# Kernel optimization log

Measured on AMD Instinct MI355X. Metric: run time of the kernel, lower is better.

## Reference

```python
import jax, jax.numpy as jnp
import numpy as np

B, LQ, LD, H, DIM, PF = 16, 64, 2048, 1024, 128, 4
MAXK = LD // PF + 1  # static upper bound on num clusters (valid_len <= LD)


def setup_inputs() -> dict:
    key = jax.random.key(0)
    k1, k2, k3, k4 = jax.random.split(key, 4)
    return {
        "q_hidden": jax.random.normal(k1, (B, LQ, H), jnp.float32),
        "d_hidden": jax.random.normal(k2, (B, LD, H), jnp.float32),
        "W": jax.random.normal(k3, (H, DIM), jnp.float32) * (1.0 / np.sqrt(H)),  # xavier-ish
        "b": jnp.zeros((DIM,), jnp.float32),
        "q_mask": jnp.ones((B, LQ), jnp.int32),
        "d_mask": jnp.ones((B, LD), jnp.int32),
        "labels": jax.random.randint(k4, (B, LD), 0, MAXK, dtype=jnp.int32),
        "pooling_factor": PF,
    }


def _encode(hidden, W, b, mask):
    # proj -> L2 normalize -> zero out padded tokens
    r = hidden @ W + b
    r = r / jnp.clip(jnp.linalg.norm(r, axis=-1, keepdims=True), 1e-12)
    return r * mask[..., None].astype(r.dtype)


def _pool(d_repr, d_mask, labels, pf):
    # segment-mean per batch sample, cluster labels supplied externally
    Bn, L, D = d_repr.shape
    max_k = L // pf + 1  # static
    valid = jnp.clip(d_mask.sum(-1), 2, None)          # [B]
    k = valid // pf + 1                                 # per-sample num clusters
    lab = jnp.where(d_mask > 0, labels % k[:, None], max_k)  # invalid tokens -> dummy seg
    seg = lambda vals, idx: jax.ops.segment_sum(vals, idx, num_segments=max_k + 1)
    sums = jax.vmap(seg)(d_repr, lab)[:, :max_k]                          # [B,K,D]
    counts = jax.vmap(seg)(jnp.where(d_mask > 0, 1.0, 0.0), lab)[:, :max_k]
    means = sums / jnp.clip(counts, 1.0)[..., None]
    means = means / jnp.clip(jnp.linalg.norm(means, axis=-1, keepdims=True), 1e-12)
    pad_mask = jnp.arange(max_k)[None, :] < k[:, None]                    # [B,K]
    return means * pad_mask[..., None], pad_mask


def reference(q_hidden, d_hidden, W, b, q_mask, d_mask, labels, pooling_factor):
    q = _encode(q_hidden, W, b, q_mask)            # [B,LQ,DIM]
    d = _encode(d_hidden, W, b, d_mask)            # [B,LD,DIM]
    d_pool, pmask = _pool(d, d_mask, labels, pooling_factor)  # [B,K,DIM]
    sim = jnp.einsum('bqd,bkd->bqk', q, d_pool)
    sim = jnp.where(pmask[:, None, :], sim, -1e4)
    score = (sim.max(-1) * q_mask.astype(sim.dtype)).sum(-1)  # maxsum per pair
    return score
```

## Files before the change

kernel.cpp:

```cpp
#include <hip/hip_runtime.h>
#include <hip/hip_bf16.h>

#define BB    16
#define LQ    64
#define LD    2048
#define HH    1024
#define DIM   128
#define MAXK  513
#define DGRID 512
#define QGRID 16
#define RSP   16

typedef __attribute__((ext_vector_type(8))) short short8;
typedef __attribute__((ext_vector_type(4))) float f32x4;

__device__ __forceinline__ float b2f(ushort u) {
    union { float f; unsigned int u32; } c; c.u32 = ((unsigned int)u) << 16; return c.f;
}
__device__ __forceinline__ ushort f2b_rn(float f) {
    unsigned int x = __float_as_uint(f);
    return (ushort)((x + 0x7fffu + ((x >> 16) & 1u)) >> 16);
}

__device__ __forceinline__ void gld16(void* lds, const void* g) {
    __builtin_amdgcn_global_load_lds(
        (const __attribute__((address_space(1))) unsigned int*)g,
        (__attribute__((address_space(3))) unsigned int*)lds,
        16, 0, 0);
}

__global__ __launch_bounds__(256) void prep_kb_kernel(
    const float* __restrict__ W,
    const int*   __restrict__ d_mask,
    const int*   __restrict__ pf,
    ushort*      __restrict__ Wt_hi,
    ushort*      __restrict__ Wt_lo,
    int*         __restrict__ kvals)
{
    __shared__ int red[4];
    int bid = blockIdx.x, t = threadIdx.x;
    if (bid < 512) {
        int idx = bid * 256 + t;
        int h = idx >> 7;
        int n = idx & 127;
        float x = W[idx];
        ushort hi = f2b_rn(x);
        float r = x - b2f(hi);
        Wt_hi[n * HH + h] = hi;
        Wt_lo[n * HH + h] = f2b_rn(r);
    } else {
        int b = bid - 512;
        int lane = t & 63, wave = t >> 6;
        int s = 0;
        for (int i = t; i < LD; i += 256) s += (d_mask[b * LD + i] > 0) ? 1 : 0;
        #pragma unroll
        for (int m = 1; m < 64; m <<= 1) s += __shfl_xor(s, m);
        if (lane == 0) red[wave] = s;
        __syncthreads();
        if (t == 0) {
            int v = red[0] + red[1] + red[2] + red[3];
            if (v < 2) v = 2;
            int pfv = pf[0];
            if (pfv < 1 || pfv > LD) pfv = 4;
            kvals[b] = v / pfv + 1;
        }
    }
}

__global__ __launch_bounds__(256, 3) void encode_kernel(
    const float*  __restrict__ Xd,
    const float*  __restrict__ Xq,
    const ushort* __restrict__ Wt_hi,
    const ushort* __restrict__ Wt_lo,
    const float*  __restrict__ bias,
    const int*    __restrict__ mask_d,
    const int*    __restrict__ mask_q,
    const int*    __restrict__ labels,
    const int*    __restrict__ kvals,
    float*        __restrict__ sums,
    float*        __restrict__ q_repr)
{
    __shared__ __align__(16) uint4 buf[2][1536];

    const int t = threadIdx.x;
    const int w = t >> 6, lane = t & 63;
    const int m16 = lane & 15, quad = lane >> 4;
    const int l8 = lane & 7, lr = lane >> 3;
    const int g = l8 ^ lr;

    const bool isq = blockIdx.x >= DGRID;
    const float* X = isq ? Xq : Xd;
    const long row0 = isq ? (long)(blockIdx.x - DGRID) * 64 : (long)blockIdx.x * 64;

    const float* gA0 = X + (row0 + w * 16 + 0 + lr) * HH + g * 4;
    const float* gA1 = X + (row0 + w * 16 + 8 + lr) * HH + g * 4;
    const ushort* bsel = (g & 4) ? Wt_lo : Wt_hi;
    const ushort* gB0 = bsel + ((w * 4 + 0) * 8 + lr) * HH + (g & 3) * 8;
    const ushort* gB1 = bsel + ((w * 4 + 1) * 8 + lr) * HH + (g & 3) * 8;
    const ushort* gB2 = bsel + ((w * 4 + 2) * 8 + lr) * HH + (g & 3) * 8;
    const ushort* gB3 = bsel + ((w * 4 + 3) * 8 + lr) * HH + (g & 3) * 8;

    f32x4 acc[8];
    #pragma unroll
    for (int j = 0; j < 8; ++j) acc[j] = (f32x4){0.f, 0.f, 0.f, 0.f};

    {
        gld16(&buf[0][(w * 2 + 0) * 64], gA0);
        gld16(&buf[0][(w * 2 + 1) * 64], gA1);
        gld16(&buf[0][512 + (w * 4 + 0) * 64], gB0);
        gld16(&buf[0][512 + (w * 4 + 1) * 64], gB1);
        gld16(&buf[0][512 + (w * 4 + 2) * 64], gB2);
        gld16(&buf[0][512 + (w * 4 + 3) * 64], gB3);
    }

    const int sw = m16 & 7;
    const int abase = (w * 16 + m16) * 8;

    for (int c = 0; c < 32; ++c) {
        __syncthreads();
        const int cur = c & 1;

        if (c < 31) {
            const int nxt = cur ^ 1;
            const int ko = (c + 1) * 32;
            gld16(&buf[nxt][(w * 2 + 0) * 64], gA0 + ko);
            gld16(&buf[nxt][(w * 2 + 1) * 64], gA1 + ko);
            gld16(&buf[nxt][512 + (w * 4 + 0) * 64], gB0 + ko);
            gld16(&buf[nxt][512 + (w * 4 + 1) * 64], gB1 + ko);
            gld16(&buf[nxt][512 + (w * 4 + 2) * 64], gB2 + ko);
            gld16(&buf[nxt][512 + (w * 4 + 3) * 64], gB3 + ko);
        }

        float4 va0 = *(const float4*)&buf[cur][abase + ((2 * quad) ^ sw)];
        float4 va1 = *(const float4*)&buf[cur][abase + ((2 * quad + 1) ^ sw)];
        float av[8];
        *(float4*)(av) = va0; *(float4*)(av + 4) = va1;
        short8 ah, al;
        #pragma unroll
        for (int j = 0; j < 8; ++j) {
            unsigned int ux = __float_as_uint(av[j]);
            ah[j] = (short)(ux >> 16);
            float hif = __uint_as_float(ux & 0xffff0000u);
            al[j] = (short)(__float_as_uint(av[j] - hif) >> 16);
        }

        #pragma unroll
        for (int ct = 0; ct < 8; ++ct) {
            const int bbase = 512 + (ct * 16 + m16) * 8;
            short8 bh = *(const short8*)&buf[cur][bbase + (quad ^ sw)];
            short8 bl = *(const short8*)&buf[cur][bbase + ((quad + 4) ^ sw)];
            acc[ct] = __builtin_amdgcn_mfma_f32_16x16x32_bf16(ah, bh, acc[ct], 0, 0, 0);
            acc[ct] = __builtin_amdgcn_mfma_f32_16x16x32_bf16(al, bh, acc[ct], 0, 0, 0);
            acc[ct] = __builtin_amdgcn_mfma_f32_16x16x32_bf16(ah, bl, acc[ct], 0, 0, 0);
        }
    }

    float bia[8];
    #pragma unroll
    for (int ct = 0; ct < 8; ++ct) bia[ct] = bias[ct * 16 + m16];

    #pragma unroll
    for (int r = 0; r < 4; ++r) {
        long rowg = row0 + w * 16 + quad * 4 + r;
        float v[8];
        float ss = 0.f;
        #pragma unroll
        for (int ct = 0; ct < 8; ++ct) {
            v[ct] = acc[ct][r] + bia[ct];
            ss += v[ct] * v[ct];
        }
        ss += __shfl_xor(ss, 1);
        ss += __shfl_xor(ss, 2);
        ss += __shfl_xor(ss, 4);
        ss += __shfl_xor(ss, 8);
        float scale = 1.0f / fmaxf(sqrtf(ss), 1e-12f);

        if (isq) {
            scale *= (float)mask_q[rowg];
            #pragma unroll
            for (int ct = 0; ct < 8; ++ct)
                q_repr[rowg * DIM + ct * 16 + m16] = v[ct] * scale;
        } else {
            if (mask_d[rowg] > 0) {
                int b = (int)(rowg >> 11);
                int seg = labels[rowg] % kvals[b];
                float* sp = sums + ((long)b * MAXK + seg) * DIM + m16;
                #pragma unroll
                for (int ct = 0; ct < 8; ++ct)
                    atomicAdd(sp + ct * 16, v[ct] * scale);
            }
        }
    }
}

__global__ __launch_bounds__(256) void simmax_kernel(
    const float* __restrict__ q_repr,
    const float* __restrict__ sums,
    const int*   __restrict__ kvals,
    const int*   __restrict__ q_mask,
    float*       __restrict__ out)
{
    __shared__ float qs[4 * 132];
    __shared__ float red[4][4];
    int b = blockIdx.x >> 4, rs = blockIdx.x & 15;
    int t = threadIdx.x, w = t >> 6, lane = t & 63;

    for (int i = t; i < 4 * DIM; i += 256) {
        int r = i >> 7, d = i & 127;
        qs[r * 132 + d] = q_repr[((long)b * LQ + rs * 4 + r) * DIM + d];
    }
    __syncthreads();

    int kb = kvals[b];
    float mx[4];
    #pragma unroll
    for (int r = 0; r < 4; ++r) mx[r] = -1e4f;

    for (int kk = t; kk < MAXK; kk += 256) {
        const float4* dp = (const float4*)(sums + ((long)b * MAXK + kk) * DIM);
        float dot[4];
        #pragma unroll
        for (int r = 0; r < 4; ++r) dot[r] = 0.f;
        float ss = 0.f;
        for (int d4 = 0; d4 < 32; ++d4) {
            float4 c = dp[d4];
            ss += c.x * c.x + c.y * c.y + c.z * c.z + c.w * c.w;
            #pragma unroll
            for (int r = 0; r < 4; ++r) {
                float4 q = *(const float4*)(&qs[r * 132 + d4 * 4]);
                dot[r] += q.x * c.x + q.y * c.y + q.z * c.z + q.w * c.w;
            }
        }
        float inv = (ss > 1e-24f) ? rsqrtf(ss) : 0.f;
        bool valid = kk < kb;
        #pragma unroll
        for (int r = 0; r < 4; ++r) {
            float sim = valid ? dot[r] * inv : -1e4f;
            mx[r] = fmaxf(mx[r], sim);
        }
    }

    #pragma unroll
    for (int r = 0; r < 4; ++r) {
        float v = mx[r];
        v = fmaxf(v, __shfl_xor(v, 1));
        v = fmaxf(v, __shfl_xor(v, 2));
        v = fmaxf(v, __shfl_xor(v, 4));
        v = fmaxf(v, __shfl_xor(v, 8));
        v = fmaxf(v, __shfl_xor(v, 16));
        v = fmaxf(v, __shfl_xor(v, 32));
        mx[r] = v;
    }
    if (lane == 0) {
        #pragma unroll
        for (int r = 0; r < 4; ++r) red[w][r] = mx[r];
    }
    __syncthreads();
    if (t < 4) {
        float m = fmaxf(fmaxf(red[0][t], red[1][t]), fmaxf(red[2][t], red[3][t]));
        m *= (float)q_mask[b * LQ + rs * 4 + t];
        atomicAdd(&out[b], m);
    }
}

extern "C" void kernel_launch(void* const* d_in, const int* in_sizes, int n_in,
                              void* d_out, int out_size, void* d_ws, size_t ws_size,
                              hipStream_t stream) {
    const float* q_hidden = (const float*)d_in[0];
    const float* d_hidden = (const float*)d_in[1];
    const float* W        = (const float*)d_in[2];
    const float* bias     = (const float*)d_in[3];
    const int*   q_mask   = (const int*)d_in[4];
    const int*   d_mask   = (const int*)d_in[5];
    const int*   labels   = (const int*)d_in[6];
    const int*   pf       = (const int*)d_in[7];

    float* ws     = (float*)d_ws;
    float* q_repr = ws;
    float* sums   = q_repr + (long)BB * LQ * DIM;
    int*   kvals  = (int*)(sums + (long)BB * MAXK * DIM);
    ushort* Wt_hi = (ushort*)(kvals + 16);
    ushort* Wt_lo = Wt_hi + (long)DIM * HH;

    hipMemsetAsync(sums, 0, (size_t)BB * MAXK * DIM * sizeof(float), stream);
    hipMemsetAsync(d_out, 0, (size_t)out_size * sizeof(float), stream);

    prep_kb_kernel<<<512 + BB, 256, 0, stream>>>(W, d_mask, pf, Wt_hi, Wt_lo, kvals);
    encode_kernel<<<DGRID + QGRID, 256, 0, stream>>>(d_hidden, q_hidden, Wt_hi, Wt_lo,
                                                     bias, d_mask, q_mask, labels, kvals,
                                                     sums, q_repr);
    simmax_kernel<<<BB * RSP, 256, 0, stream>>>(q_repr, sums, kvals, q_mask, (float*)d_out);
}
```

Measured before the change: 291.5 us.

## Drop W low-part split, shrink encode tiles, and move simmax to MFMA

W is now kept as a single bf16 copy, so each k-step of the encode GEMM issues two MFMAs instead of three. The encode tile drops to 32 rows, which doubles the grid and raises the occupancy target to 4 blocks, and the row norm is combined through shared memory. The similarity-max stage becomes a bf16 MFMA GEMM over 64-cluster chunks with split-precision queries, writing partial maxima that a small final kernel reduces without atomics. Dropping W's low part and quantising the cluster sums to bf16 lowers precision and may put error near the tolerance.

```diff
diff --git a/kernel.cpp b/kernel.cpp
--- a/kernel.cpp
+++ b/kernel.cpp
@@ -7,9 +7,9 @@
 #define HH    1024
 #define DIM   128
 #define MAXK  513
-#define DGRID 512
-#define QGRID 16
-#define RSP   16
+#define SCH   9
+#define DGRID 1024
+#define QGRID 32
 
 typedef __attribute__((ext_vector_type(8))) short short8;
 typedef __attribute__((ext_vector_type(4))) float f32x4;
@@ -33,8 +33,7 @@
     const float* __restrict__ W,
     const int*   __restrict__ d_mask,
     const int*   __restrict__ pf,
-    ushort*      __restrict__ Wt_hi,
-    ushort*      __restrict__ Wt_lo,
+    ushort*      __restrict__ Wt,
     int*         __restrict__ kvals)
 {
     __shared__ int red[4];
@@ -43,11 +42,7 @@
         int idx = bid * 256 + t;
         int h = idx >> 7;
         int n = idx & 127;
-        float x = W[idx];
-        ushort hi = f2b_rn(x);
-        float r = x - b2f(hi);
-        Wt_hi[n * HH + h] = hi;
-        Wt_lo[n * HH + h] = f2b_rn(r);
+        Wt[n * HH + h] = f2b_rn(W[idx]);
     } else {
         int b = bid - 512;
         int lane = t & 63, wave = t >> 6;
@@ -67,11 +62,10 @@
     }
 }
 
-__global__ __launch_bounds__(256, 3) void encode_kernel(
+__global__ __launch_bounds__(256, 4) void encode_kernel(
     const float*  __restrict__ Xd,
     const float*  __restrict__ Xq,
-    const ushort* __restrict__ Wt_hi,
-    const ushort* __restrict__ Wt_lo,
+    const ushort* __restrict__ Wt,
     const float*  __restrict__ bias,
     const int*    __restrict__ mask_d,
     const int*    __restrict__ mask_q,
@@ -80,41 +74,36 @@
     float*        __restrict__ sums,
     float*        __restrict__ q_repr)
 {
-    __shared__ __align__(16) uint4 buf[2][1536];
+    __shared__ __align__(16) uint4 buf[2][768];
+    __shared__ float ssh[32][2];
+
+    const int bid = blockIdx.x;
+    const bool isq = bid >= DGRID;
+    const float* X = isq ? Xq : Xd;
+    const long row0 = isq ? (long)(bid - DGRID) * 32 : (long)bid * 32;
 
     const int t = threadIdx.x;
     const int w = t >> 6, lane = t & 63;
     const int m16 = lane & 15, quad = lane >> 4;
-    const int l8 = lane & 7, lr = lane >> 3;
-    const int g = l8 ^ lr;
-
-    const bool isq = blockIdx.x >= DGRID;
-    const float* X = isq ? Xq : Xd;
-    const long row0 = isq ? (long)(blockIdx.x - DGRID) * 64 : (long)blockIdx.x * 64;
-
-    const float* gA0 = X + (row0 + w * 16 + 0 + lr) * HH + g * 4;
-    const float* gA1 = X + (row0 + w * 16 + 8 + lr) * HH + g * 4;
-    const ushort* bsel = (g & 4) ? Wt_lo : Wt_hi;
-    const ushort* gB0 = bsel + ((w * 4 + 0) * 8 + lr) * HH + (g & 3) * 8;
-    const ushort* gB1 = bsel + ((w * 4 + 1) * 8 + lr) * HH + (g & 3) * 8;
-    const ushort* gB2 = bsel + ((w * 4 + 2) * 8 + lr) * HH + (g & 3) * 8;
-    const ushort* gB3 = bsel + ((w * 4 + 3) * 8 + lr) * HH + (g & 3) * 8;
-
-    f32x4 acc[8];
-    #pragma unroll
-    for (int j = 0; j < 8; ++j) acc[j] = (f32x4){0.f, 0.f, 0.f, 0.f};
-
-    {
-        gld16(&buf[0][(w * 2 + 0) * 64], gA0);
-        gld16(&buf[0][(w * 2 + 1) * 64], gA1);
-        gld16(&buf[0][512 + (w * 4 + 0) * 64], gB0);
-        gld16(&buf[0][512 + (w * 4 + 1) * 64], gB1);
-        gld16(&buf[0][512 + (w * 4 + 2) * 64], gB2);
-        gld16(&buf[0][512 + (w * 4 + 3) * 64], gB3);
-    }
+    const int rh = w & 1, ch = w >> 1;
+
+    const float*  gA  = X + (row0 + w * 8 + (lane >> 3)) * HH
+                          + (((lane & 7) ^ ((lane >> 3) & 7)) * 4);
+    const ushort* gB0 = Wt + (long)(w * 32 + (lane >> 2)) * HH
+                           + (((lane & 3) ^ ((lane >> 4) & 3)) * 8);
+    const ushort* gB1 = gB0 + 16 * HH;
+
+    f32x4 acc[4];
+    #pragma unroll
+    for (int j = 0; j < 4; ++j) acc[j] = (f32x4){0.f, 0.f, 0.f, 0.f};
+
+    gld16(&buf[0][w * 64], gA);
+    gld16(&buf[0][256 + w * 128], gB0);
+    gld16(&buf[0][256 + w * 128 + 64], gB1);
 
     const int sw = m16 & 7;
-    const int abase = (w * 16 + m16) * 8;
+    const int bsw = m16 >> 2;
+    const int au = (rh * 16 + m16) * 8;
 
     for (int c = 0; c < 32; ++c) {
         __syncthreads();
@@ -123,16 +112,13 @@
         if (c < 31) {
             const int nxt = cur ^ 1;
             const int ko = (c + 1) * 32;
-            gld16(&buf[nxt][(w * 2 + 0) * 64], gA0 + ko);
-            gld16(&buf[nxt][(w * 2 + 1) * 64], gA1 + ko);
-            gld16(&buf[nxt][512 + (w * 4 + 0) * 64], gB0 + ko);
-            gld16(&buf[nxt][512 + (w * 4 + 1) * 64], gB1 + ko);
-            gld16(&buf[nxt][512 + (w * 4 + 2) * 64], gB2 + ko);
-            gld16(&buf[nxt][512 + (w * 4 + 3) * 64], gB3 + ko);
-        }
-
-        float4 va0 = *(const float4*)&buf[cur][abase + ((2 * quad) ^ sw)];
-        float4 va1 = *(const float4*)&buf[cur][abase + ((2 * quad + 1) ^ sw)];
+            gld16(&buf[nxt][w * 64], gA + ko);
+            gld16(&buf[nxt][256 + w * 128], gB0 + ko);
+            gld16(&buf[nxt][256 + w * 128 + 64], gB1 + ko);
+        }
+
+        float4 va0 = *(const float4*)&buf[cur][au + ((2 * quad) ^ sw)];
+        float4 va1 = *(const float4*)&buf[cur][au + ((2 * quad + 1) ^ sw)];
         float av[8];
         *(float4*)(av) = va0; *(float4*)(av + 4) = va1;
         short8 ah, al;
@@ -145,50 +131,58 @@
         }
 
         #pragma unroll
-        for (int ct = 0; ct < 8; ++ct) {
-            const int bbase = 512 + (ct * 16 + m16) * 8;
-            short8 bh = *(const short8*)&buf[cur][bbase + (quad ^ sw)];
-            short8 bl = *(const short8*)&buf[cur][bbase + ((quad + 4) ^ sw)];
-            acc[ct] = __builtin_amdgcn_mfma_f32_16x16x32_bf16(ah, bh, acc[ct], 0, 0, 0);
-            acc[ct] = __builtin_amdgcn_mfma_f32_16x16x32_bf16(al, bh, acc[ct], 0, 0, 0);
-            acc[ct] = __builtin_amdgcn_mfma_f32_16x16x32_bf16(ah, bl, acc[ct], 0, 0, 0);
-        }
-    }
-
-    float bia[8];
-    #pragma unroll
-    for (int ct = 0; ct < 8; ++ct) bia[ct] = bias[ct * 16 + m16];
-
+        for (int cti = 0; cti < 4; ++cti) {
+            const int ct = ch * 4 + cti;
+            short8 bf = *(const short8*)&buf[cur][256 + (ct * 16 + m16) * 4 + (quad ^ bsw)];
+            acc[cti] = __builtin_amdgcn_mfma_f32_16x16x32_bf16(ah, bf, acc[cti], 0, 0, 0);
+            acc[cti] = __builtin_amdgcn_mfma_f32_16x16x32_bf16(al, bf, acc[cti], 0, 0, 0);
+        }
+    }
+
+    float bia[4];
+    #pragma unroll
+    for (int cti = 0; cti < 4; ++cti) bia[cti] = bias[(ch * 4 + cti) * 16 + m16];
+
+    float vv[4][4];
+    float ssp[4] = {0.f, 0.f, 0.f, 0.f};
+    #pragma unroll
+    for (int cti = 0; cti < 4; ++cti)
+        #pragma unroll
+        for (int r = 0; r < 4; ++r) {
+            vv[cti][r] = acc[cti][r] + bia[cti];
+            ssp[r] += vv[cti][r] * vv[cti][r];
+        }
     #pragma unroll
     for (int r = 0; r < 4; ++r) {
-        long rowg = row0 + w * 16 + quad * 4 + r;
-        float v[8];
-        float ss = 0.f;
-        #pragma unroll
-        for (int ct = 0; ct < 8; ++ct) {
-            v[ct] = acc[ct][r] + bia[ct];
-            ss += v[ct] * v[ct];
-        }
-        ss += __shfl_xor(ss, 1);
-        ss += __shfl_xor(ss, 2);
-        ss += __shfl_xor(ss, 4);
-        ss += __shfl_xor(ss, 8);
+        ssp[r] += __shfl_xor(ssp[r], 1);
+        ssp[r] += __shfl_xor(ssp[r], 2);
+        ssp[r] += __shfl_xor(ssp[r], 4);
+        ssp[r] += __shfl_xor(ssp[r], 8);
+    }
+    if (m16 == 0) {
+        #pragma unroll
+        for (int r = 0; r < 4; ++r) ssh[rh * 16 + quad * 4 + r][ch] = ssp[r];
+    }
+    __syncthreads();
+
+    #pragma unroll
+    for (int r = 0; r < 4; ++r) {
+        int rowl = rh * 16 + quad * 4 + r;
+        long rowg = row0 + rowl;
+        float ss = ssh[rowl][0] + ssh[rowl][1];
         float scale = 1.0f / fmaxf(sqrtf(ss), 1e-12f);
-
         if (isq) {
             scale *= (float)mask_q[rowg];
             #pragma unroll
-            for (int ct = 0; ct < 8; ++ct)
-                q_repr[rowg * DIM + ct * 16 + m16] = v[ct] * scale;
-        } else {
-            if (mask_d[rowg] > 0) {
-                int b = (int)(rowg >> 11);
-                int seg = labels[rowg] % kvals[b];
-                float* sp = sums + ((long)b * MAXK + seg) * DIM + m16;
-                #pragma unroll
-                for (int ct = 0; ct < 8; ++ct)
-                    atomicAdd(sp + ct * 16, v[ct] * scale);
-            }
+            for (int cti = 0; cti < 4; ++cti)
+                q_repr[rowg * DIM + (ch * 4 + cti) * 16 + m16] = vv[cti][r] * scale;
+        } else if (mask_d[rowg] > 0) {
+            int b = (int)(rowg >> 11);
+            int seg = labels[rowg] % kvals[b];
+            float* sp = sums + ((long)b * MAXK + seg) * DIM + m16;
+            #pragma unroll
+            for (int cti = 0; cti < 4; ++cti)
+                atomicAdd(sp + (ch * 4 + cti) * 16, vv[cti][r] * scale);
         }
     }
 }
@@ -197,70 +191,113 @@
     const float* __restrict__ q_repr,
     const float* __restrict__ sums,
     const int*   __restrict__ kvals,
+    float*       __restrict__ pmax)
+{
+    __shared__ __align__(16) ushort Qh[64 * 136];
+    __shared__ __align__(16) ushort Ql[64 * 136];
+    __shared__ __align__(16) ushort Ch[64 * 136];
+    __shared__ float cn[64];
+
+    int b = blockIdx.x / SCH, chunk = blockIdx.x % SCH;
+    int t = threadIdx.x, w = t >> 6, lane = t & 63;
+    int m16 = lane & 15, quad = lane >> 4;
+
+    #pragma unroll
+    for (int i = 0; i < 8; ++i) {
+        int flat = i * 256 + t;
+        int row = flat >> 5, c4 = flat & 31;
+        float4 v = *(const float4*)(q_repr + ((long)b * LQ + row) * DIM + c4 * 4);
+        float x[4]; *(float4*)x = v;
+        ushort4 h, l;
+        ushort* hp = (ushort*)&h; ushort* lp = (ushort*)&l;
+        #pragma unroll
+        for (int j = 0; j < 4; ++j) {
+            unsigned int ux = __float_as_uint(x[j]);
+            hp[j] = (ushort)(ux >> 16);
+            lp[j] = f2b_rn(x[j] - __uint_as_float(ux & 0xffff0000u));
+        }
+        *(ushort4*)&Qh[row * 136 + c4 * 4] = h;
+        *(ushort4*)&Ql[row * 136 + c4 * 4] = l;
+    }
+    #pragma unroll
+    for (int i = 0; i < 8; ++i) {
+        int flat = i * 256 + t;
+        int row = flat >> 5, c4 = flat & 31;
+        int kk = chunk * 64 + row;
+        float4 v = (kk < MAXK)
+            ? *(const float4*)(sums + ((long)b * MAXK + kk) * DIM + c4 * 4)
+            : make_float4(0.f, 0.f, 0.f, 0.f);
+        ushort4 h; ushort* hp = (ushort*)&h;
+        hp[0] = f2b_rn(v.x); hp[1] = f2b_rn(v.y);
+        hp[2] = f2b_rn(v.z); hp[3] = f2b_rn(v.w);
+        *(ushort4*)&Ch[row * 136 + c4 * 4] = h;
+    }
+    __syncthreads();
+
+    {
+        int c = w * 16 + m16;
+        float ssv = 0.f;
+        #pragma unroll
+        for (int j = 0; j < 16; ++j) {
+            unsigned int u = *(const unsigned int*)&Ch[c * 136 + quad * 32 + j * 2];
+            float x0 = b2f((ushort)u), x1 = b2f((ushort)(u >> 16));
+            ssv += x0 * x0 + x1 * x1;
+        }
+        ssv += __shfl_xor(ssv, 16);
+        ssv += __shfl_xor(ssv, 32);
+        if (quad == 0) cn[c] = (ssv > 1e-24f) ? rsqrtf(ssv) : 0.f;
+    }
+    __syncthreads();
+
+    f32x4 acc[4];
+    #pragma unroll
+    for (int j = 0; j < 4; ++j) acc[j] = (f32x4){0.f, 0.f, 0.f, 0.f};
+
+    #pragma unroll
+    for (int kc = 0; kc < 4; ++kc) {
+        short8 qh = *(const short8*)&Qh[(w * 16 + m16) * 136 + kc * 32 + quad * 8];
+        short8 ql = *(const short8*)&Ql[(w * 16 + m16) * 136 + kc * 32 + quad * 8];
+        #pragma unroll
+        for (int ct = 0; ct < 4; ++ct) {
+            short8 cf = *(const short8*)&Ch[(ct * 16 + m16) * 136 + kc * 32 + quad * 8];
+            acc[ct] = __builtin_amdgcn_mfma_f32_16x16x32_bf16(qh, cf, acc[ct], 0, 0, 0);
+            acc[ct] = __builtin_amdgcn_mfma_f32_16x16x32_bf16(ql, cf, acc[ct], 0, 0, 0);
+        }
+    }
+
+    int kb = kvals[b];
+    #pragma unroll
+    for (int r = 0; r < 4; ++r) {
+        float mx = -1e4f;
+        #pragma unroll
+        for (int ct = 0; ct < 4; ++ct) {
+            int cl = chunk * 64 + ct * 16 + m16;
+            float sim = acc[ct][r] * cn[ct * 16 + m16];
+            mx = fmaxf(mx, (cl < kb) ? sim : -1e4f);
+        }
+        mx = fmaxf(mx, __shfl_xor(mx, 1));
+        mx = fmaxf(mx, __shfl_xor(mx, 2));
+        mx = fmaxf(mx, __shfl_xor(mx, 4));
+        mx = fmaxf(mx, __shfl_xor(mx, 8));
+        if (m16 == 0)
+            pmax[((long)b * SCH + chunk) * 64 + w * 16 + quad * 4 + r] = mx;
+    }
+}
+
+__global__ __launch_bounds__(64) void final_kernel(
+    const float* __restrict__ pmax,
     const int*   __restrict__ q_mask,
     float*       __restrict__ out)
 {
-    __shared__ float qs[4 * 132];
-    __shared__ float red[4][4];
-    int b = blockIdx.x >> 4, rs = blockIdx.x & 15;
-    int t = threadIdx.x, w = t >> 6, lane = t & 63;
-
-    for (int i = t; i < 4 * DIM; i += 256) {
-        int r = i >> 7, d = i & 127;
-        qs[r * 132 + d] = q_repr[((long)b * LQ + rs * 4 + r) * DIM + d];
-    }
-    __syncthreads();
-
-    int kb = kvals[b];
-    float mx[4];
-    #pragma unroll
-    for (int r = 0; r < 4; ++r) mx[r] = -1e4f;
-
-    for (int kk = t; kk < MAXK; kk += 256) {
-        const float4* dp = (const float4*)(sums + ((long)b * MAXK + kk) * DIM);
-        float dot[4];
-        #pragma unroll
-        for (int r = 0; r < 4; ++r) dot[r] = 0.f;
-        float ss = 0.f;
-        for (int d4 = 0; d4 < 32; ++d4) {
-            float4 c = dp[d4];
-            ss += c.x * c.x + c.y * c.y + c.z * c.z + c.w * c.w;
-            #pragma unroll
-            for (int r = 0; r < 4; ++r) {
-                float4 q = *(const float4*)(&qs[r * 132 + d4 * 4]);
-                dot[r] += q.x * c.x + q.y * c.y + q.z * c.z + q.w * c.w;
-            }
-        }
-        float inv = (ss > 1e-24f) ? rsqrtf(ss) : 0.f;
-        bool valid = kk < kb;
-        #pragma unroll
-        for (int r = 0; r < 4; ++r) {
-            float sim = valid ? dot[r] * inv : -1e4f;
-            mx[r] = fmaxf(mx[r], sim);
-        }
-    }
-
-    #pragma unroll
-    for (int r = 0; r < 4; ++r) {
-        float v = mx[r];
-        v = fmaxf(v, __shfl_xor(v, 1));
-        v = fmaxf(v, __shfl_xor(v, 2));
-        v = fmaxf(v, __shfl_xor(v, 4));
-        v = fmaxf(v, __shfl_xor(v, 8));
-        v = fmaxf(v, __shfl_xor(v, 16));
-        v = fmaxf(v, __shfl_xor(v, 32));
-        mx[r] = v;
-    }
-    if (lane == 0) {
-        #pragma unroll
-        for (int r = 0; r < 4; ++r) red[w][r] = mx[r];
-    }
-    __syncthreads();
-    if (t < 4) {
-        float m = fmaxf(fmaxf(red[0][t], red[1][t]), fmaxf(red[2][t], red[3][t]));
-        m *= (float)q_mask[b * LQ + rs * 4 + t];
-        atomicAdd(&out[b], m);
-    }
+    int b = blockIdx.x, r = threadIdx.x;
+    float m = -3e38f;
+    #pragma unroll
+    for (int c = 0; c < SCH; ++c)
+        m = fmaxf(m, pmax[((long)b * SCH + c) * 64 + r]);
+    m *= (float)q_mask[b * LQ + r];
+    #pragma unroll
+    for (int sh = 1; sh < 64; sh <<= 1) m += __shfl_xor(m, sh);
+    if (r == 0) out[b] = m;
 }
 
 extern "C" void kernel_launch(void* const* d_in, const int* in_sizes, int n_in,
@@ -278,16 +315,16 @@
     float* ws     = (float*)d_ws;
     float* q_repr = ws;
     float* sums   = q_repr + (long)BB * LQ * DIM;
-    int*   kvals  = (int*)(sums + (long)BB * MAXK * DIM);
-    ushort* Wt_hi = (ushort*)(kvals + 16);
-    ushort* Wt_lo = Wt_hi + (long)DIM * HH;
+    float* pmaxb  = sums + (long)BB * MAXK * DIM;
+    int*   kvals  = (int*)(pmaxb + BB * SCH * 64);
+    ushort* Wt    = (ushort*)(kvals + 16);
 
     hipMemsetAsync(sums, 0, (size_t)BB * MAXK * DIM * sizeof(float), stream);
-    hipMemsetAsync(d_out, 0, (size_t)out_size * sizeof(float), stream);
-
-    prep_kb_kernel<<<512 + BB, 256, 0, stream>>>(W, d_mask, pf, Wt_hi, Wt_lo, kvals);
-    encode_kernel<<<DGRID + QGRID, 256, 0, stream>>>(d_hidden, q_hidden, Wt_hi, Wt_lo,
-                                                     bias, d_mask, q_mask, labels, kvals,
+
+    prep_kb_kernel<<<512 + BB, 256, 0, stream>>>(W, d_mask, pf, Wt, kvals);
+    encode_kernel<<<DGRID + QGRID, 256, 0, stream>>>(d_hidden, q_hidden, Wt, bias,
+                                                     d_mask, q_mask, labels, kvals,
                                                      sums, q_repr);
-    simmax_kernel<<<BB * RSP, 256, 0, stream>>>(q_repr, sums, kvals, q_mask, (float*)d_out);
-}
+    simmax_kernel<<<BB * SCH, 256, 0, stream>>>(q_repr, sums, kvals, pmaxb);
+    final_kernel<<<BB, 64, 0, stream>>>(pmaxb, q_mask, (float*)d_out);
+}
```

New measurement: 256.9 us. 11.9% less time.
